# Optimization experiments

Measured on AMD Instinct MI355X. Metric: run time of the kernel, lower is better.

The kernel has to match this reference:

```python
import jax, jax.numpy as jnp
import numpy as np

C_IN, C_INT = 256, 128


def setup_inputs() -> dict:
    key = jax.random.key(0)
    ks = jax.random.split(key, 7)
    B, H, W = 8, 64, 64
    s_in = 1.0 / np.sqrt(C_IN)
    return {
        "x": jax.random.normal(ks[0], (B, C_IN, H, W), dtype=jnp.float32),
        "w_theta": jax.random.uniform(ks[1], (C_INT, C_IN), jnp.float32, -s_in, s_in),
        "b_theta": jax.random.uniform(ks[2], (C_INT,), jnp.float32, -s_in, s_in),
        "w_phi": jax.random.uniform(ks[3], (C_INT, C_IN), jnp.float32, -s_in, s_in),
        "b_phi": jax.random.uniform(ks[4], (C_INT,), jnp.float32, -s_in, s_in),
        "w_g": jax.random.uniform(ks[5], (C_INT, C_IN), jnp.float32, -s_in, s_in),
        "b_g": jax.random.uniform(ks[6], (C_INT,), jnp.float32, -s_in, s_in),
    }


def reference(x, w_theta, b_theta, w_phi, b_phi, w_g, b_g):
    B, C, H, W = x.shape
    # flatten spatial: [B, N, C], 1x1 conv == per-position linear
    xf = x.reshape(B, C, H * W).transpose(0, 2, 1)  # [B, N, C_in]
    theta = jnp.einsum('bnc,dc->bnd', xf, w_theta) + b_theta  # [B, N, C_int]
    phi = jnp.einsum('bnc,dc->bnd', xf, w_phi) + b_phi        # [B, N, C_int]
    g = jnp.einsum('bnc,dc->bnd', xf, w_g) + b_g              # [B, N, C_int]
    f = jnp.einsum('bnd,bmd->bnm', theta, phi)  # [B, N, N] unscaled scores
    f_div_C = jax.nn.softmax(f, axis=-1)
    y = jnp.einsum('bnm,bmd->bnd', f_div_C, g)  # [B, N, C_int]
    # back to [B, C_int, H, W]
    return y.transpose(0, 2, 1).reshape(B, C_INT, H, W)
```

## Files before the change

kernel.cpp:

```cpp
#include <hip/hip_runtime.h>

typedef __attribute__((ext_vector_type(8))) short bf8;
typedef __attribute__((ext_vector_type(4))) float f4;
typedef unsigned short u16;

constexpr int B_ = 8, CIN = 256, CINT = 128, NN = 4096;
constexpr float L2E = 1.44269504088896f;

__device__ __forceinline__ u16 f2bf(float f) {
  unsigned int u = __builtin_bit_cast(unsigned int, f);
  u += 0x7FFFu + ((u >> 16) & 1u);
  return (u16)(u >> 16);
}

__device__ __forceinline__ void glds16(const void* g, void* l) {
  __builtin_amdgcn_global_load_lds(
      (const __attribute__((address_space(1))) unsigned int*)g,
      (__attribute__((address_space(3))) unsigned int*)l, 16, 0, 0);
}

__device__ __forceinline__ int cvtpk(float lo, float hi) {
  int r;
  asm("v_cvt_pk_bf16_f32 %0, %1, %2" : "=v"(r) : "v"(lo), "v"(hi));
  return r;
}

__global__ __launch_bounds__(256) void prep_kernel(
    const float* __restrict__ wth, const float* __restrict__ wph,
    const float* __restrict__ wg, u16* __restrict__ wbf)
{
  int i = blockIdx.x * 256 + threadIdx.x;
  const float* src = (i < 32768) ? wth : (i < 65536) ? wph : wg;
  wbf[i] = f2bf(src[i & 32767]);
}

__global__ __launch_bounds__(256) void proj_kernel(
    const float* __restrict__ x, const u16* __restrict__ wbf,
    const float* __restrict__ bth, const float* __restrict__ bph,
    const float* __restrict__ bg,
    u16* __restrict__ theta, u16* __restrict__ phiT, u16* __restrict__ gTt)
{
  const int b = blockIdx.y, n0 = blockIdx.x * 64;
  const int tid = threadIdx.x, w = tid >> 6, l = tid & 63;
  const int lr = l & 15, lg = l >> 4;
  __shared__ __align__(16) u16 sx[64 * 256];

  const float* xb = x + (size_t)b * CIN * NN + n0;
  #pragma unroll
  for (int pass = 0; pass < 8; ++pass) {
    const int cb = w * 8 + pass * 32;
    u16 tmp[8];
    #pragma unroll
    for (int i = 0; i < 8; ++i) tmp[i] = f2bf(xb[(size_t)(cb + i) * NN + l]);
    uint4 v;
    v.x = (unsigned)tmp[0] | ((unsigned)tmp[1] << 16);
    v.y = (unsigned)tmp[2] | ((unsigned)tmp[3] << 16);
    v.z = (unsigned)tmp[4] | ((unsigned)tmp[5] << 16);
    v.w = (unsigned)tmp[6] | ((unsigned)tmp[7] << 16);
    *(uint4*)&sx[l * 256 + (((w + pass * 4) ^ (l & 7)) << 3)] = v;
  }
  __syncthreads();

  #pragma unroll
  for (int dti = 0; dti < 6; ++dti) {
    const int dt = w * 6 + dti;
    const int mat = dt >> 3, d0 = (dt & 7) * 16;
    const float* Bv = (mat == 0) ? bth : (mat == 1) ? bph : bg;
    const u16* wrow = wbf + mat * 32768 + (size_t)(d0 + lr) * 256 + lg * 8;
    bf8 wf[8];
    #pragma unroll
    for (int ks = 0; ks < 8; ++ks) wf[ks] = *(const bf8*)(wrow + ks * 32);

    #pragma unroll
    for (int mt = 0; mt < 4; ++mt) {
      f4 acc = {0.f, 0.f, 0.f, 0.f};
      const int row = mt * 16 + lr;
      #pragma unroll
      for (int ks = 0; ks < 8; ++ks) {
        bf8 bx = *(const bf8*)&sx[row * 256 + (((ks * 4 + lg) ^ (lr & 7)) << 3)];
        acc = __builtin_amdgcn_mfma_f32_16x16x32_bf16(wf[ks], bx, acc, 0, 0, 0);
      }
      const int m = n0 + mt * 16 + lr;
      const int dlo = d0 + lg * 4;
      if (mat == 0) {
        ushort4 h4;
        h4.x = f2bf(acc[0] + Bv[dlo + 0]);
        h4.y = f2bf(acc[1] + Bv[dlo + 1]);
        h4.z = f2bf(acc[2] + Bv[dlo + 2]);
        h4.w = f2bf(acc[3] + Bv[dlo + 3]);
        *(ushort4*)&theta[((size_t)b * NN + m) * CINT + dlo] = h4;
      } else if (mat == 1) {
        const int kt = m >> 5, r32 = m & 31;
        ushort4 h4;
        h4.x = f2bf((acc[0] + Bv[dlo + 0]) * L2E);
        h4.y = f2bf((acc[1] + Bv[dlo + 1]) * L2E);
        h4.z = f2bf((acc[2] + Bv[dlo + 2]) * L2E);
        h4.w = f2bf((acc[3] + Bv[dlo + 3]) * L2E);
        *(ushort4*)&phiT[((size_t)(b * 128 + kt)) * 4096 + r32 * 128 +
                         ((((dlo >> 3) ^ (r32 & 7))) << 3) + (dlo & 7)] = h4;
      } else {
        const int kt = m >> 5, kk = m & 31;
        #pragma unroll
        for (int r = 0; r < 4; ++r) {
          const int d = dlo + r;
          const int grow = d >> 1;
          const int chunk = (((d & 1) * 4 + (kk >> 3)) ^ (grow & 7));
          gTt[((size_t)(b * 128 + kt)) * 4096 + grow * 64 + chunk * 8 + (kk & 7)]
              = f2bf(acc[r] + Bv[d]);
        }
      }
    }
  }
}

__global__ __launch_bounds__(512, 2) void attn_kernel(
    const u16* __restrict__ theta, const u16* __restrict__ phiT,
    const u16* __restrict__ gTt, float* __restrict__ out)
{
  const int b  = blockIdx.y;
  const int t_ = threadIdx.x;
  const int w  = t_ >> 6;
  const int l  = t_ & 63;
  const int lr = l & 15, lg = l >> 4;
  const int h  = w >> 2, wq = w & 3;
  const int qw = blockIdx.x * 128 + wq * 32;

  __shared__ __align__(16) char smem[67584];
  u16* sphi_b = (u16*)smem;
  u16* sg_b   = (u16*)(smem + 32768);

  const u16* th = theta + (size_t)b * NN * CINT;
  bf8 qf[2][4];
  #pragma unroll
  for (int qt = 0; qt < 2; ++qt)
    #pragma unroll
    for (int ds = 0; ds < 4; ++ds)
      qf[qt][ds] = *(const bf8*)(th + (size_t)(qw + qt * 16 + lr) * CINT + ds * 32 + lg * 8);

  f4 y[2][8];
  #pragma unroll
  for (int qt = 0; qt < 2; ++qt)
    #pragma unroll
    for (int dt = 0; dt < 8; ++dt) y[qt][dt] = (f4){0.f, 0.f, 0.f, 0.f};
  float rs[2] = {0.f, 0.f};

  const char* psrc = (const char*)(phiT + (size_t)(b * 128 + h * 64) * 4096) +
                     wq * 2048 + l * 16;
  const char* gsrc = (const char*)(gTt + (size_t)(b * 128 + h * 64) * 4096) +
                     wq * 2048 + l * 16;

  #define STAGE(BUF, T)                                                    \
    {                                                                      \
      const char* sp = psrc + (size_t)(T) * 8192;                          \
      const char* sq = gsrc + (size_t)(T) * 8192;                          \
      char* lp = (char*)(sphi_b + (h * 2 + (BUF)) * 4096) + wq * 2048;     \
      char* lq = (char*)(sg_b + (h * 2 + (BUF)) * 4096) + wq * 2048;       \
      glds16(sp, lp); glds16(sp + 1024, lp + 1024);                        \
      glds16(sq, lq); glds16(sq + 1024, lq + 1024);                        \
    }

  STAGE(0, 0);
  asm volatile("s_waitcnt vmcnt(0)" ::: "memory");
  __builtin_amdgcn_s_barrier();
  __builtin_amdgcn_sched_barrier(0);

  int cur = 0;
  for (int t = 0; t < 64; ++t) {
    if (t < 63) STAGE(cur ^ 1, t + 1);

    const u16* PH = sphi_b + (h * 2 + cur) * 4096;
    const u16* GG = sg_b + (h * 2 + cur) * 4096;

    f4 s[2][2];
    s[0][0] = (f4){0.f,0.f,0.f,0.f}; s[0][1] = (f4){0.f,0.f,0.f,0.f};
    s[1][0] = (f4){0.f,0.f,0.f,0.f}; s[1][1] = (f4){0.f,0.f,0.f,0.f};
    __builtin_amdgcn_s_setprio(1);
    #pragma unroll
    for (int st = 0; st < 2; ++st) {
      const u16* base = PH + (st * 16 + lr) * 128;
      #pragma unroll
      for (int ds = 0; ds < 4; ++ds) {
        bf8 af = *(const bf8*)(base + (((ds * 4 + lg) ^ (lr & 7)) << 3));
        s[0][st] = __builtin_amdgcn_mfma_f32_16x16x32_bf16(af, qf[0][ds], s[0][st], 0, 0, 0);
        s[1][st] = __builtin_amdgcn_mfma_f32_16x16x32_bf16(af, qf[1][ds], s[1][st], 0, 0, 0);
      }
    }
    __builtin_amdgcn_s_setprio(0);

    bf8 gfr[8];
    #pragma unroll
    for (int dt = 0; dt < 8; ++dt) {
      const int grow = dt * 8 + (lr >> 1);
      const int chunk = (((lr & 1) * 4 + lg) ^ (grow & 7));
      gfr[dt] = *(const bf8*)(GG + grow * 64 + chunk * 8);
    }

    #pragma unroll
    for (int qt = 0; qt < 2; ++qt) {
      float p0 = __builtin_amdgcn_exp2f(s[qt][0][0]);
      float p1 = __builtin_amdgcn_exp2f(s[qt][0][1]);
      float p2 = __builtin_amdgcn_exp2f(s[qt][0][2]);
      float p3 = __builtin_amdgcn_exp2f(s[qt][0][3]);
      float p4 = __builtin_amdgcn_exp2f(s[qt][1][0]);
      float p5 = __builtin_amdgcn_exp2f(s[qt][1][1]);
      float p6 = __builtin_amdgcn_exp2f(s[qt][1][2]);
      float p7 = __builtin_amdgcn_exp2f(s[qt][1][3]);
      rs[qt] += ((p0 + p1) + (p2 + p3)) + ((p4 + p5) + (p6 + p7));

      int w0 = cvtpk(p0, p1), w1 = cvtpk(p2, p3);
      int w2 = cvtpk(p4, p5), w3 = cvtpk(p6, p7);
      asm volatile("v_permlane32_swap_b32 %0, %1" : "+v"(w0), "+v"(w2));
      asm volatile("v_permlane16_swap_b32 %0, %1" : "+v"(w0), "+v"(w2));
      asm volatile("v_permlane32_swap_b32 %0, %1" : "+v"(w1), "+v"(w3));
      asm volatile("v_permlane16_swap_b32 %0, %1" : "+v"(w1), "+v"(w3));
      int pai[4] = {w0, w1, w2, w3};
      bf8 paf = __builtin_bit_cast(bf8, *(int4*)pai);

      __builtin_amdgcn_s_setprio(1);
      #pragma unroll
      for (int dt = 0; dt < 8; ++dt)
        y[qt][dt] = __builtin_amdgcn_mfma_f32_16x16x32_bf16(paf, gfr[dt], y[qt][dt], 0, 0, 0);
      __builtin_amdgcn_s_setprio(0);
    }

    if (t < 63) asm volatile("s_waitcnt vmcnt(0)" ::: "memory");
    __builtin_amdgcn_s_barrier();
    __builtin_amdgcn_sched_barrier(0);
    cur ^= 1;
  }

  #pragma unroll
  for (int qt = 0; qt < 2; ++qt) {
    rs[qt] += __shfl_xor(rs[qt], 16);
    rs[qt] += __shfl_xor(rs[qt], 32);
  }
  __syncthreads();
  float* ycomb  = (float*)smem;
  float* rscomb = (float*)(smem + 65536);
  if (h == 1) {
    #pragma unroll
    for (int qt = 0; qt < 2; ++qt) {
      #pragma unroll
      for (int dt = 0; dt < 8; ++dt)
        *(f4*)&ycomb[wq * 4096 + (qt * 8 + dt) * 256 + l * 4] = y[qt][dt];
      rscomb[wq * 128 + qt * 64 + l] = rs[qt];
    }
  }
  __syncthreads();
  if (h == 0) {
    #pragma unroll
    for (int qt = 0; qt < 2; ++qt) {
      #pragma unroll
      for (int dt = 0; dt < 8; ++dt)
        y[qt][dt] += *(const f4*)&ycomb[wq * 4096 + (qt * 8 + dt) * 256 + l * 4];
      rs[qt] += rscomb[wq * 128 + qt * 64 + l];
    }
    float* ob = out + (size_t)b * CINT * NN;
    #pragma unroll
    for (int qt = 0; qt < 2; ++qt) {
      f4 rsi;
      #pragma unroll
      for (int r = 0; r < 4; ++r)
        rsi[r] = 1.0f / __shfl(rs[qt], lg * 4 + r, 64);
      #pragma unroll
      for (int dt = 0; dt < 8; ++dt) {
        f4 v = y[qt][dt] * rsi;
        *(float4*)&ob[(size_t)(dt * 16 + lr) * NN + qw + qt * 16 + lg * 4] = *(float4*)&v;
      }
    }
  }
}

extern "C" void kernel_launch(void* const* d_in, const int* in_sizes, int n_in,
                              void* d_out, int out_size, void* d_ws, size_t ws_size,
                              hipStream_t stream) {
  const float* x   = (const float*)d_in[0];
  const float* wth = (const float*)d_in[1];
  const float* bth = (const float*)d_in[2];
  const float* wph = (const float*)d_in[3];
  const float* bph = (const float*)d_in[4];
  const float* wg  = (const float*)d_in[5];
  const float* bg  = (const float*)d_in[6];
  float* out = (float*)d_out;

  u16* theta = (u16*)d_ws;
  u16* phiT  = theta + (size_t)B_ * NN * CINT;
  u16* gTt   = phiT  + (size_t)B_ * NN * CINT;
  u16* wbf   = gTt   + (size_t)B_ * NN * CINT;

  hipLaunchKernelGGL(prep_kernel, dim3(384), dim3(256), 0, stream, wth, wph, wg, wbf);
  hipLaunchKernelGGL(proj_kernel, dim3(64, 8), dim3(256), 0, stream,
                     x, wbf, bth, bph, bg, theta, phiT, gTt);
  hipLaunchKernelGGL(attn_kernel, dim3(32, 8), dim3(512), 0, stream,
                     theta, phiT, gTt, out);
}
```

Before: 104.7 us.

## Halve attention block size to 64 queries and interleave batch across block ids

```diff
diff --git a/kernel.cpp b/kernel.cpp
--- a/kernel.cpp
+++ b/kernel.cpp
@@ -113,19 +113,21 @@
   }
 }
 
-__global__ __launch_bounds__(512, 2) void attn_kernel(
+__global__ __launch_bounds__(256, 2) void attn_kernel(
     const u16* __restrict__ theta, const u16* __restrict__ phiT,
     const u16* __restrict__ gTt, float* __restrict__ out)
 {
-  const int b  = blockIdx.y;
+  const int bid = blockIdx.x;
+  const int b   = bid & 7;
+  const int qtl = bid >> 3;
   const int t_ = threadIdx.x;
   const int w  = t_ >> 6;
   const int l  = t_ & 63;
   const int lr = l & 15, lg = l >> 4;
-  const int h  = w >> 2, wq = w & 3;
-  const int qw = blockIdx.x * 128 + wq * 32;
-
-  __shared__ __align__(16) char smem[67584];
+  const int qs = w & 1, h = w >> 1;
+  const int q0 = qtl * 64 + qs * 32;
+
+  __shared__ __align__(16) char smem[66560];
   u16* sphi_b = (u16*)smem;
   u16* sg_b   = (u16*)(smem + 32768);
 
@@ -135,7 +137,7 @@
   for (int qt = 0; qt < 2; ++qt)
     #pragma unroll
     for (int ds = 0; ds < 4; ++ds)
-      qf[qt][ds] = *(const bf8*)(th + (size_t)(qw + qt * 16 + lr) * CINT + ds * 32 + lg * 8);
+      qf[qt][ds] = *(const bf8*)(th + (size_t)(q0 + qt * 16 + lr) * CINT + ds * 32 + lg * 8);
 
   f4 y[2][8];
   #pragma unroll
@@ -145,18 +147,20 @@
   float rs[2] = {0.f, 0.f};
 
   const char* psrc = (const char*)(phiT + (size_t)(b * 128 + h * 64) * 4096) +
-                     wq * 2048 + l * 16;
+                     qs * 1024 + l * 16;
   const char* gsrc = (const char*)(gTt + (size_t)(b * 128 + h * 64) * 4096) +
-                     wq * 2048 + l * 16;
-
-  #define STAGE(BUF, T)                                                    \
-    {                                                                      \
-      const char* sp = psrc + (size_t)(T) * 8192;                          \
-      const char* sq = gsrc + (size_t)(T) * 8192;                          \
-      char* lp = (char*)(sphi_b + (h * 2 + (BUF)) * 4096) + wq * 2048;     \
-      char* lq = (char*)(sg_b + (h * 2 + (BUF)) * 4096) + wq * 2048;       \
-      glds16(sp, lp); glds16(sp + 1024, lp + 1024);                        \
-      glds16(sq, lq); glds16(sq + 1024, lq + 1024);                        \
+                     qs * 1024 + l * 16;
+
+  #define STAGE(BUF, T)                                                     \
+    {                                                                       \
+      const char* sp = psrc + (size_t)(T) * 8192;                           \
+      const char* sq = gsrc + (size_t)(T) * 8192;                           \
+      char* lp = (char*)sphi_b + (h * 2 + (BUF)) * 8192 + qs * 1024;        \
+      char* lq = (char*)sg_b + (h * 2 + (BUF)) * 8192 + qs * 1024;          \
+      glds16(sp, lp);               glds16(sp + 2048, lp + 2048);           \
+      glds16(sp + 4096, lp + 4096); glds16(sp + 6144, lp + 6144);           \
+      glds16(sq, lq);               glds16(sq + 2048, lq + 2048);           \
+      glds16(sq + 4096, lq + 4096); glds16(sq + 6144, lq + 6144);           \
     }
 
   STAGE(0, 0);
@@ -192,7 +196,7 @@
     for (int dt = 0; dt < 8; ++dt) {
       const int grow = dt * 8 + (lr >> 1);
       const int chunk = (((lr & 1) * 4 + lg) ^ (grow & 7));
-      gfr[dt] = *(const bf8*)(GG + grow * 64 + chunk * 8);
+      gfr[dt] = *(const bf8*)(GG + grow * 64 + (chunk << 3));
     }
 
     #pragma unroll
@@ -223,7 +227,7 @@
       __builtin_amdgcn_s_setprio(0);
     }
 
-    if (t < 63) asm volatile("s_waitcnt vmcnt(0)" ::: "memory");
+    asm volatile("s_waitcnt vmcnt(0)" ::: "memory");
     __builtin_amdgcn_s_barrier();
     __builtin_amdgcn_sched_barrier(0);
     cur ^= 1;
@@ -235,15 +239,15 @@
     rs[qt] += __shfl_xor(rs[qt], 32);
   }
   __syncthreads();
-  float* ycomb  = (float*)smem;
-  float* rscomb = (float*)(smem + 65536);
+  float* yc = (float*)smem;
+  float* rc = (float*)(smem + 65536);
   if (h == 1) {
     #pragma unroll
     for (int qt = 0; qt < 2; ++qt) {
       #pragma unroll
       for (int dt = 0; dt < 8; ++dt)
-        *(f4*)&ycomb[wq * 4096 + (qt * 8 + dt) * 256 + l * 4] = y[qt][dt];
-      rscomb[wq * 128 + qt * 64 + l] = rs[qt];
+        *(f4*)&yc[qs * 4096 + (qt * 8 + dt) * 256 + l * 4] = y[qt][dt];
+      rc[qs * 128 + qt * 64 + l] = rs[qt];
     }
   }
   __syncthreads();
@@ -252,8 +256,8 @@
     for (int qt = 0; qt < 2; ++qt) {
       #pragma unroll
       for (int dt = 0; dt < 8; ++dt)
-        y[qt][dt] += *(const f4*)&ycomb[wq * 4096 + (qt * 8 + dt) * 256 + l * 4];
-      rs[qt] += rscomb[wq * 128 + qt * 64 + l];
+        y[qt][dt] += *(const f4*)&yc[qs * 4096 + (qt * 8 + dt) * 256 + l * 4];
+      rs[qt] += rc[qs * 128 + qt * 64 + l];
     }
     float* ob = out + (size_t)b * CINT * NN;
     #pragma unroll
@@ -265,7 +269,7 @@
       #pragma unroll
       for (int dt = 0; dt < 8; ++dt) {
         f4 v = y[qt][dt] * rsi;
-        *(float4*)&ob[(size_t)(dt * 16 + lr) * NN + qw + qt * 16 + lg * 4] = *(float4*)&v;
+        *(float4*)&ob[(size_t)(dt * 16 + lr) * NN + q0 + qt * 16 + lg * 4] = *(float4*)&v;
       }
     }
   }
@@ -291,6 +295,6 @@
   hipLaunchKernelGGL(prep_kernel, dim3(384), dim3(256), 0, stream, wth, wph, wg, wbf);
   hipLaunchKernelGGL(proj_kernel, dim3(64, 8), dim3(256), 0, stream,
                      x, wbf, bth, bph, bg, theta, phiT, gTt);
-  hipLaunchKernelGGL(attn_kernel, dim3(32, 8), dim3(512), 0, stream,
+  hipLaunchKernelGGL(attn_kernel, dim3(512), dim3(256), 0, stream,
                      theta, phiT, gTt, out);
 }
```

New measurement: 110.7 us. 5.7% more time.
